# Kernel tuning notes

Hardware: AMD Instinct MI355X
Metric: run time of the kernel (lower is better)

## Reference

```python
import jax, jax.numpy as jnp
import numpy as np
import math

B, T, C, H, S = 2, 2048, 1024, 16, 16
HD = C // H
EPS = 1e-5


def setup_inputs() -> dict:
    key = jax.random.key(0)
    ks = jax.random.split(key, 20)
    sc = 1.0 / math.sqrt(C)
    inp = {
        "x": jax.random.normal(ks[0], (B, T, C), jnp.float32),
        # A_log_fwd: log(arange(1..S)) repeated over dim (as in __init__)
        "A_log": jnp.log(jnp.tile(jnp.arange(1, S + 1, dtype=jnp.float32), (C, 1))),
        # Linear weights stored (in, out); apply as x @ W + b
        "Wd": jax.random.normal(ks[1], (C, C), jnp.float32) * sc,
        "bd": jnp.full((C,), -3.0, jnp.float32),
        "WB": jax.random.normal(ks[2], (C, S), jnp.float32) * sc,
        "WC": jax.random.normal(ks[3], (C, S), jnp.float32) * sc,
        "Wq": jax.random.normal(ks[4], (C, C), jnp.float32) * sc,
        "bq": jnp.zeros((C,), jnp.float32),
        "Wk": jax.random.normal(ks[5], (C, C), jnp.float32) * sc,
        "bk": jnp.zeros((C,), jnp.float32),
        "Wv": jax.random.normal(ks[6], (C, C), jnp.float32) * sc,
        "bv": jnp.zeros((C,), jnp.float32),
        "Wx": jax.random.normal(ks[7], (C, C), jnp.float32) * sc,
        "bx": jnp.zeros((C,), jnp.float32),
        "Wo": jax.random.normal(ks[8], (C, C), jnp.float32) * sc,
        "bo": jnp.zeros((C,), jnp.float32),
        "ln_g": jnp.ones((C,), jnp.float32),
        "ln_b": jnp.zeros((C,), jnp.float32),
        "temp": jnp.full((1, H, 1, 1), 0.5, jnp.float32),
    }
    return inp


def _forward(x, A_log, Wd, bd, WB, WC, Wq, bq, Wk, bk, Wv, bv, Wx, bx, Wo, bo, ln_g, ln_b, temp):
    x_base = x @ Wx + bx                      # (B,T,C)
    delta = jax.nn.softplus(x @ Wd + bd)      # (B,T,C)
    B_mat = x @ WB                            # (B,T,S)
    C_mat = x @ WC                            # (B,T,S)
    A = -jnp.exp(A_log)                       # (C,S)

    def scan_fn(h, inp):
        xb_t, d_t, B_t, C_t = inp             # (B,C),(B,C),(B,S),(B,S)
        bar_A = jnp.exp(d_t[..., None] * A)   # (B,C,S)
        h = bar_A * h + (d_t * xb_t)[..., None] * B_t[:, None, :]
        y = jnp.einsum('bcs,bs->bc', h, C_t)
        return h, y

    h0 = jnp.zeros((B, C, S), x.dtype)
    xs = (jnp.swapaxes(x_base, 0, 1), jnp.swapaxes(delta, 0, 1),
          jnp.swapaxes(B_mat, 0, 1), jnp.swapaxes(C_mat, 0, 1))
    _, ys = jax.lax.scan(scan_fn, h0, xs)
    out_fwd = jnp.swapaxes(ys, 0, 1)          # (B,T,C)

    # LayerNorm(x_base + out_fwd)
    hyb = x_base + out_fwd
    mu = hyb.mean(-1, keepdims=True)
    var = hyb.var(-1, keepdims=True)
    hybrid = (hyb - mu) * jax.lax.rsqrt(var + EPS) * ln_g + ln_b

    def heads(W, b):
        return (hybrid @ W + b).reshape(B, T, H, HD).transpose(0, 2, 1, 3)

    Q, K, V = heads(Wq, bq), heads(Wk, bk), heads(Wv, bv)
    scores = jnp.einsum('bhqd,bhkd->bhqk', Q, K) / math.sqrt(HD)
    scores = scores * jax.nn.softplus(temp)
    mask = jnp.tril(jnp.ones((T, T), bool))
    scores = jnp.where(mask[None, None], scores, -jnp.inf)
    attn = jax.nn.softmax(scores, axis=-1)
    out = jnp.einsum('bhqk,bhkd->bhqd', attn, V).transpose(0, 2, 1, 3).reshape(B, T, C)
    return out @ Wo + bo


def reference(x, A_log, Wd, bd, WB, WC, Wq, bq, Wk, bk, Wv, bv, Wx, bx, Wo, bo, ln_g, ln_b, temp):
    return _forward(x, A_log, Wd, bd, WB, WC, Wq, bq, Wk, bk, Wv, bv, Wx, bx, Wo, bo, ln_g, ln_b, temp)
```

## Files before the change

### kernel.cpp

```cpp
#include <hip/hip_runtime.h>
#include <math.h>

#define B_  2
#define T_  2048
#define C_  1024
#define H_  16
#define S_  16
#define HD_ 64
#define NCH 32
#define CHL 64

typedef short  short8  __attribute__((ext_vector_type(8)));
typedef unsigned short ushort8 __attribute__((ext_vector_type(8)));
typedef unsigned short ushort4v __attribute__((ext_vector_type(4)));
typedef float  f32x4   __attribute__((ext_vector_type(4)));

__device__ __forceinline__ float softplus_f(float v) {
    return fmaxf(v, 0.f) + log1pf(__expf(-fabsf(v)));
}

__device__ __forceinline__ unsigned short f2bf(float x) {
    unsigned u = __float_as_uint(x);
    u += 0x7fffu + ((u >> 16) & 1u);
    return (unsigned short)(u >> 16);
}

__device__ __forceinline__ void gload16(const unsigned short* g,
                                        unsigned short* l)
{
    __builtin_amdgcn_global_load_lds(
        (const __attribute__((address_space(1))) unsigned int*)g,
        (__attribute__((address_space(3))) unsigned int*)l, 16, 0, 0);
}

__global__ __launch_bounds__(256) void cast_bf16(const float* __restrict__ in,
                                                 unsigned short* __restrict__ out,
                                                 int n4)
{
    int i = blockIdx.x * 256 + threadIdx.x;
    if (i >= n4) return;
    float4 v = ((const float4*)in)[i];
    ushort4v o = {f2bf(v.x), f2bf(v.y), f2bf(v.z), f2bf(v.w)};
    ((ushort4v*)out)[i] = o;
}

__device__ __forceinline__ void wtrans_body(const float* __restrict__ W,
                                            unsigned short* __restrict__ WT,
                                            int bx, int by, int tid)
{
    __shared__ float t[32][33];
    const int n0 = bx * 32, k0 = by * 32;
    const int tx = tid & 31, ty = tid >> 5;
#pragma unroll
    for (int p = 0; p < 4; ++p)
        t[ty + p * 8][tx] = W[(size_t)(k0 + ty + p * 8) * C_ + n0 + tx];
    __syncthreads();
#pragma unroll
    for (int p = 0; p < 4; ++p)
        WT[(size_t)(n0 + ty + p * 8) * C_ + k0 + tx] = f2bf(t[tx][ty + p * 8]);
}

__global__ __launch_bounds__(256) void wtrans(const float* __restrict__ W,
                                              unsigned short* __restrict__ WT)
{
    wtrans_body(W, WT, blockIdx.x, blockIdx.y, threadIdx.x);
}

__global__ __launch_bounds__(256) void wtrans_multi(
    const float* __restrict__ Wx, const float* __restrict__ Wd,
    const float* __restrict__ Wq, const float* __restrict__ Wk,
    const float* __restrict__ Wv,
    unsigned short* __restrict__ Astack, unsigned short* __restrict__ Wqkv)
{
    const float* src;
    unsigned short* dst;
    switch (blockIdx.z) {
        case 0: src = Wx; dst = Astack; break;
        case 1: src = Wd; dst = Astack + (size_t)1024 * 1024; break;
        case 2: src = Wq; dst = Wqkv; break;
        case 3: src = Wk; dst = Wqkv + (size_t)1024 * 1024; break;
        default: src = Wv; dst = Wqkv + (size_t)2048 * 1024; break;
    }
    wtrans_body(src, dst, blockIdx.x, blockIdx.y, threadIdx.x);
}

__global__ __launch_bounds__(256) void prep_misc(
    const float* __restrict__ WB, const float* __restrict__ WC,
    const float* __restrict__ bx, const float* __restrict__ bd,
    const float* __restrict__ bq, const float* __restrict__ bk,
    const float* __restrict__ bv,
    unsigned short* __restrict__ Astack, float* __restrict__ biasPD,
    float* __restrict__ biasQKV)
{
    int gid = blockIdx.x * 256 + threadIdx.x;
    if (gid < 32768) {
        int w = gid >> 14, rem = gid & 16383;
        int s = rem >> 10, k = rem & 1023;
        const float* src = w ? WC : WB;
        Astack[(size_t)(2048 + w * 16 + s) * 1024 + k] = f2bf(src[k * 16 + s]);
    } else {
        int id = gid - 32768;
        if (id < 2176) {
            biasPD[id] = id < 1024 ? bx[id] : (id < 2048 ? bd[id - 1024] : 0.f);
        } else {
            int id2 = id - 2176;
            if (id2 < 3072)
                biasQKV[id2] = id2 < 1024 ? bq[id2]
                             : (id2 < 2048 ? bk[id2 - 1024] : bv[id2 - 2048]);
        }
    }
}

__global__ __launch_bounds__(256) void gemm_mfma(
    const unsigned short* __restrict__ A, const unsigned short* __restrict__ Bm,
    const float* __restrict__ bias,
    void* __restrict__ outv,
    int M, int N, int K, int lda)
{
    __shared__ __align__(16) unsigned short As[4][4096];
    __shared__ __align__(16) unsigned short Bs[4][4096];

    const int tid = threadIdx.x;
    const int w = tid >> 6, lane = tid & 63;
    const int lq = lane & 15, lg = lane >> 4;
    const int wm = w >> 1, wn = w & 1;
    const int mBase = blockIdx.y * 128, nBase = blockIdx.x * 128;

    const int c0 = tid, c1 = tid + 256;
    const int rA0 = ((c0 >> 6) << 4) + (c0 & 15), kO0 = ((c0 >> 4) & 3) << 3;
    const int rA1 = ((c1 >> 6) << 4) + (c1 & 15), kO1 = ((c1 >> 4) & 3) << 3;

    const int wL0 = w * 512;
    const int wL1 = 2048 + w * 512;

    f32x4 acc[4][4];
#pragma unroll
    for (int i = 0; i < 4; ++i)
#pragma unroll
        for (int j = 0; j < 4; ++j) acc[i][j] = (f32x4){0.f, 0.f, 0.f, 0.f};

    const unsigned short* ga0 = A  + (size_t)(mBase + rA0) * lda + kO0;
    const unsigned short* ga1 = A  + (size_t)(mBase + rA1) * lda + kO1;
    const unsigned short* gb0 = Bm + (size_t)(nBase + rA0) * lda + kO0;
    const unsigned short* gb1 = Bm + (size_t)(nBase + rA1) * lda + kO1;

    #define STAGE(bufv, k0v)                               \
        do {                                               \
            gload16(ga0 + (k0v), &As[bufv][wL0]);          \
            gload16(ga1 + (k0v), &As[bufv][wL1]);          \
            gload16(gb0 + (k0v), &Bs[bufv][wL0]);          \
            gload16(gb1 + (k0v), &Bs[bufv][wL1]);          \
        } while (0)
    #define COMPUTE(bufv)                                                       \
        do {                                                                    \
            short8 a[4], b[4];                                                  \
            _Pragma("unroll")                                                   \
            for (int i = 0; i < 4; ++i)                                         \
                a[i] = *(const short8*)&As[bufv][((wm * 4 + i) * 64 + lg * 16 + lq) * 8]; \
            _Pragma("unroll")                                                   \
            for (int j = 0; j < 4; ++j)                                         \
                b[j] = *(const short8*)&Bs[bufv][((wn * 4 + j) * 64 + lg * 16 + lq) * 8]; \
            _Pragma("unroll")                                                   \
            for (int i = 0; i < 4; ++i)                                         \
                _Pragma("unroll")                                               \
                for (int j = 0; j < 4; ++j)                                     \
                    acc[i][j] = __builtin_amdgcn_mfma_f32_16x16x32_bf16(        \
                        a[i], b[j], acc[i][j], 0, 0, 0);                        \
        } while (0)
    #define WAITV4() asm volatile("s_waitcnt vmcnt(4)" ::: "memory")
    #define WAITV0() asm volatile("s_waitcnt vmcnt(0)" ::: "memory")
    #define LGKM0()  asm volatile("s_waitcnt lgkmcnt(0)" ::: "memory")
    #define STEP(cbuf, kt)                                          \
        do {                                                        \
            if ((kt) + 32 < K) WAITV4(); else WAITV0();             \
            LGKM0();                                                \
            __builtin_amdgcn_s_barrier();                           \
            if ((kt) + 64 < K) STAGE(((cbuf) + 2) & 3, (kt) + 64);  \
            COMPUTE(cbuf);                                          \
        } while (0)

    STAGE(0, 0);
    STAGE(1, 32);

    for (int k0 = 0; k0 < K; k0 += 128) {
        STEP(0, k0);
        STEP(1, k0 + 32);
        STEP(2, k0 + 64);
        STEP(3, k0 + 96);
    }
    #undef STAGE
    #undef COMPUTE
    #undef WAITV4
    #undef WAITV0
    #undef LGKM0
    #undef STEP

    float* O = (float*)outv;
#pragma unroll
    for (int j = 0; j < 4; ++j) {
        int Cg = nBase + wn * 64 + j * 16 + lq;
        float bb = bias[Cg];
#pragma unroll
        for (int i = 0; i < 4; ++i) {
            int Rb = mBase + wm * 64 + i * 16 + lg * 4;
#pragma unroll
            for (int r = 0; r < 4; ++r)
                O[(size_t)(Rb + r) * N + Cg] = acc[i][j][r] + bb;
        }
    }
}

__global__ __launch_bounds__(512, 2) void gemm_projT(
    const unsigned short* __restrict__ A, const unsigned short* __restrict__ Bm,
    const float* __restrict__ bias,
    float* __restrict__ xbaseT, float* __restrict__ deltaT,
    float* __restrict__ BmT, float* __restrict__ CmT,
    int K, int lda)
{
    __shared__ __align__(16) unsigned short AS[2][2][4096];
    __shared__ __align__(16) unsigned short BS[2][2][8192];

    const int tid = threadIdx.x;
    const int w = tid >> 6, lane = tid & 63;
    const int lq = lane & 15, lg = lane >> 4;
    const int wm = w >> 2, wn = w & 3;
    const int mBase = blockIdx.y * 128, nBase = blockIdx.x * 256;

    const int rA = ((tid >> 6) << 4) | (tid & 15);
    const int kA = ((tid >> 4) & 3) << 3;
    const unsigned short* gA = A + (size_t)(mBase + rA) * lda + kA;
    const int eA = tid * 8;
    const int c0 = tid, c1 = tid + 512;
    const int rB0 = ((c0 >> 6) << 4) | (c0 & 15), kB0 = ((c0 >> 4) & 3) << 3;
    const int rB1 = ((c1 >> 6) << 4) | (c1 & 15), kB1 = ((c1 >> 4) & 3) << 3;
    const unsigned short* gB0 = Bm + (size_t)(nBase + rB0) * lda + kB0;
    const unsigned short* gB1 = Bm + (size_t)(nBase + rB1) * lda + kB1;

    f32x4 acc[4][4];
#pragma unroll
    for (int i = 0; i < 4; ++i)
#pragma unroll
        for (int j = 0; j < 4; ++j) acc[i][j] = (f32x4){0.f, 0.f, 0.f, 0.f};

    #define STG(buf_, half_, kb_)                                             \
        do {                                                                  \
            gload16(gA  + (kb_) + (half_) * 32, &AS[buf_][half_][eA]);        \
            gload16(gB0 + (kb_) + (half_) * 32, &BS[buf_][half_][c0 * 8]);    \
            gload16(gB1 + (kb_) + (half_) * 32, &BS[buf_][half_][c1 * 8]);    \
        } while (0)
    #define WAITV6() asm volatile("s_waitcnt vmcnt(6)" ::: "memory")
    #define WAITV3() asm volatile("s_waitcnt vmcnt(3)" ::: "memory")
    #define WAITV0() asm volatile("s_waitcnt vmcnt(0)" ::: "memory")

    #define PHASE(buf_, half_, STAGE_STMT, GATE_STMT)                         \
        do {                                                                  \
            short8 a_[4], b_[4];                                              \
            _Pragma("unroll")                                                 \
            for (int i = 0; i < 4; ++i)                                       \
                a_[i] = *(const short8*)&AS[buf_][half_]                      \
                    [((wm * 4 + i) * 64 + lg * 16 + lq) * 8];                 \
            _Pragma("unroll")                                                 \
            for (int j = 0; j < 4; ++j)                                       \
                b_[j] = *(const short8*)&BS[buf_][half_]                      \
                    [((wn * 4 + j) * 64 + lg * 16 + lq) * 8];                 \
            STAGE_STMT;                                                       \
            __builtin_amdgcn_s_barrier();                                     \
            asm volatile("s_waitcnt lgkmcnt(0)" ::: "memory");                \
            __builtin_amdgcn_s_setprio(1);                                    \
            _Pragma("unroll")                                                 \
            for (int i = 0; i < 4; ++i)                                       \
                _Pragma("unroll")                                             \
                for (int j = 0; j < 4; ++j)                                   \
                    acc[i][j] = __builtin_amdgcn_mfma_f32_16x16x32_bf16(      \
                        a_[i], b_[j], acc[i][j], 0, 0, 0);                    \
            __builtin_amdgcn_s_setprio(0);                                    \
            GATE_STMT;                                                        \
            __builtin_amdgcn_s_barrier();                                     \
        } while (0)

    STG(0, 0, 0);
    STG(0, 1, 0);
    STG(1, 0, 64);
    WAITV6();
    __builtin_amdgcn_s_barrier();

    const int NT = K >> 6;
    for (int kt = 0; kt < NT; ++kt) {
        const int buf = kt & 1, nbuf = buf ^ 1;
        const int kb1 = (kt + 1) << 6, kb2 = (kt + 2) << 6;
        PHASE(buf, 0, { if (kt + 1 < NT) STG(nbuf, 1, kb1); },
              { if (kt < NT - 1) WAITV6(); else WAITV3(); });
        PHASE(buf, 1, { if (kt + 2 < NT) STG(buf, 0, kb2); },
              { if (kt < NT - 2) WAITV6();
                else if (kt == NT - 2) WAITV3(); else WAITV0(); });
    }
    #undef STG
    #undef WAITV6
    #undef WAITV3
    #undef WAITV0
    #undef PHASE

#pragma unroll
    for (int i = 0; i < 4; ++i) {
        int Rb = mBase + wm * 64 + i * 16 + lg * 4;
        if (Rb >= 2080) continue;
        float bb[4];
#pragma unroll
        for (int r = 0; r < 4; ++r) bb[r] = bias[Rb + r];
#pragma unroll
        for (int j = 0; j < 4; ++j) {
            int Cg = nBase + wn * 64 + j * 16 + lq;
            int b = Cg >> 11, t = Cg & (T_ - 1);
#pragma unroll
            for (int r = 0; r < 4; ++r) {
                int R = Rb + r;
                float v = acc[i][j][r] + bb[r];
                if (Rb < 1024) {
                    xbaseT[((size_t)b * C_ + R) * T_ + t] = v;
                } else if (Rb < 2048) {
                    deltaT[((size_t)b * C_ + (R - 1024)) * T_ + t] =
                        softplus_f(v);
                } else if (Rb < 2064) {
                    BmT[((size_t)b * S_ + (R - 2048)) * T_ + t] = v;
                } else {
                    CmT[((size_t)b * S_ + (R - 2064)) * T_ + t] = v;
                }
            }
        }
    }
}

__global__ __launch_bounds__(512, 2) void gemm_mfma256(
    const unsigned short* __restrict__ A, const unsigned short* __restrict__ Bm,
    const float* __restrict__ bias,
    void* __restrict__ outv, void* __restrict__ out2,
    void* __restrict__ out3,
    int M, int N, int K, int lda)
{
    __shared__ __align__(16) unsigned short AS[2][2][8192];
    __shared__ __align__(16) unsigned short BS[2][2][8192];

    const int tid = threadIdx.x;
    const int w = tid >> 6, lane = tid & 63;
    const int lq = lane & 15, lg = lane >> 4;
    const int wm = w >> 2, wn = w & 3;
    const int mBase = blockIdx.y * 256, nBase = blockIdx.x * 256;

    const int c0 = tid, c1 = tid + 512;
    const int r0 = ((c0 >> 6) << 4) | (c0 & 15), k0l = ((c0 >> 4) & 3) << 3;
    const int r1 = ((c1 >> 6) << 4) | (c1 & 15), k1l = ((c1 >> 4) & 3) << 3;
    const unsigned short* gA0 = A  + (size_t)(mBase + r0) * lda + k0l;
    const unsigned short* gA1 = A  + (size_t)(mBase + r1) * lda + k1l;
    const unsigned short* gB0 = Bm + (size_t)(nBase + r0) * lda + k0l;
    const unsigned short* gB1 = Bm + (size_t)(nBase + r1) * lda + k1l;

    f32x4 acc[8][4];
#pragma unroll
    for (int i = 0; i < 8; ++i)
#pragma unroll
        for (int j = 0; j < 4; ++j) acc[i][j] = (f32x4){0.f, 0.f, 0.f, 0.f};

    #define STG_A(buf_, half_, kb_)                                           \
        do {                                                                  \
            gload16(gA0 + (kb_) + (half_) * 32, &AS[buf_][half_][c0 * 8]);    \
            gload16(gA1 + (kb_) + (half_) * 32, &AS[buf_][half_][c1 * 8]);    \
        } while (0)
    #define STG_B(buf_, half_, kb_)                                           \
        do {                                                                  \
            gload16(gB0 + (kb_) + (half_) * 32, &BS[buf_][half_][c0 * 8]);    \
            gload16(gB1 + (kb_) + (half_) * 32, &BS[buf_][half_][c1 * 8]);    \
        } while (0)
    #define WAITV8() asm volatile("s_waitcnt vmcnt(8)" ::: "memory")
    #define WAITV4() asm volatile("s_waitcnt vmcnt(4)" ::: "memory")
    #define WAITV0() asm volatile("s_waitcnt vmcnt(0)" ::: "memory")

    #define PHASE(buf_, half_, qi_, STAGE_STMT, GATE_STMT)                    \
        do {                                                                  \
            short8 a_[4];                                                     \
            _Pragma("unroll")                                                 \
            for (int i = 0; i < 4; ++i)                                       \
                a_[i] = *(const short8*)&AS[buf_][half_]                      \
                    [((wm * 8 + (qi_) * 4 + i) * 64 + lg * 16 + lq) * 8];     \
            if ((qi_) == 0) {                                                 \
                _Pragma("unroll")                                             \
                for (int j = 0; j < 4; ++j)                                   \
                    bfr[j] = *(const short8*)&BS[buf_][half_]                 \
                        [((wn * 4 + j) * 64 + lg * 16 + lq) * 8];             \
            }                                                                 \
            STAGE_STMT;                                                       \
            __builtin_amdgcn_s_barrier();                                     \
            asm volatile("s_waitcnt lgkmcnt(0)" ::: "memory");                \
            __builtin_amdgcn_s_setprio(1);                                    \
            _Pragma("unroll")                                                 \
            for (int i = 0; i < 4; ++i)                                       \
                _Pragma("unroll")                                             \
                for (int j = 0; j < 4; ++j)                                   \
                    acc[(qi_) * 4 + i][j] =                                   \
                        __builtin_amdgcn_mfma_f32_16x16x32_bf16(              \
                            a_[i], bfr[j], acc[(qi_) * 4 + i][j], 0, 0, 0);   \
            __builtin_amdgcn_s_setprio(0);                                    \
            GATE_STMT;                                                        \
            __builtin_amdgcn_s_barrier();                                     \
        } while (0)

    STG_A(0, 0, 0);
    STG_B(0, 0, 0);
    STG_A(0, 1, 0);
    STG_B(0, 1, 0);
    STG_A(1, 0, 64);
    STG_B(1, 0, 64);
    WAITV8();
    __builtin_amdgcn_s_barrier();

    const int NT = K >> 6;
    for (int kt = 0; kt < NT; ++kt) {
        const int buf = kt & 1, nbuf = buf ^ 1;
        const int kb1 = (kt + 1) << 6, kb2 = (kt + 2) << 6;
        short8 bfr[4];
        PHASE(buf, 0, 0, { if (kt + 1 < NT) STG_A(nbuf, 1, kb1); }, {});
        PHASE(buf, 0, 1, { if (kt + 1 < NT) STG_B(nbuf, 1, kb1); },
              { if (kt < NT - 1) WAITV8(); else WAITV0(); });
        PHASE(buf, 1, 0, { if (kt + 2 < NT) STG_A(buf, 0, kb2); }, {});
        PHASE(buf, 1, 1, { if (kt + 2 < NT) STG_B(buf, 0, kb2); },
              { if (kt < NT - 2) WAITV8();
                else if (kt == NT - 2) WAITV4(); });
    }
    #undef STG_A
    #undef STG_B
    #undef WAITV8
    #undef WAITV4
    #undef WAITV0
    #undef PHASE

    unsigned short* Qb  = (unsigned short*)outv;
    unsigned short* Kb  = (unsigned short*)out2;
    unsigned short* VTb = (unsigned short*)out3;
#pragma unroll
    for (int j = 0; j < 4; ++j) {
        int Cg = nBase + wn * 64 + j * 16 + lq;
        int reg = Cg >> 10, c = Cg & 1023;
        int h = c >> 6, hd = c & 63;
        float bb = bias[Cg];
#pragma unroll
        for (int i = 0; i < 8; ++i) {
            int Rb = mBase + wm * 128 + i * 16 + lg * 4;
#pragma unroll
            for (int r = 0; r < 4; ++r) {
                int R = Rb + r, b = R >> 11, t = R & (T_ - 1);
                unsigned short o = f2bf(acc[i][j][r] + bb);
                if (reg == 0)
                    Qb[(((size_t)(b * H_ + h) * T_ + t) * HD_) + hd] = o;
                else if (reg == 1)
                    Kb[(((size_t)(b * H_ + h) * T_ + t) * HD_) + hd] = o;
                else
                    VTb[(((size_t)(b * H_ + h) * HD_ + hd) * T_) + t] = o;
            }
        }
    }
}

__global__ __launch_bounds__(256) void scan_partial(
    const float* __restrict__ xbaseT, const float* __restrict__ deltaT,
    const float* __restrict__ BmT, const float* __restrict__ A_log,
    float4* __restrict__ Pbuf, float4* __restrict__ Lbuf)
{
    const int tid = threadIdx.x;
    const int s4 = tid & 3;
    const int cm = tid >> 2;
    const int cg = blockIdx.x & 15;
    const int k  = (blockIdx.x >> 4) & (NCH - 1);
    const int b  = blockIdx.x >> 9;
    const int c  = cg * 64 + cm;

    float a[4];
#pragma unroll
    for (int j = 0; j < 4; ++j)
        a[j] = -__expf(A_log[c * S_ + s4 * 4 + j]);

    const int tb = k * CHL;
    const float* dp = deltaT + ((size_t)b * C_ + c) * T_ + tb;
    const float* xp = xbaseT + ((size_t)b * C_ + c) * T_ + tb;
    const float* bp = BmT + ((size_t)(b * S_ + s4 * 4)) * T_ + tb;

    float L[4] = {0.f, 0.f, 0.f, 0.f};
    float sumd = 0.f;

    float4 d4 = *(const float4*)&dp[0];
    float4 x4 = *(const float4*)&xp[0];
    float4 b4[4];
#pragma unroll
    for (int j = 0; j < 4; ++j) b4[j] = *(const float4*)&bp[(size_t)j * T_];

    for (int t0 = 0; t0 < CHL; t0 += 4) {
        const int tn = (t0 + 4 < CHL) ? t0 + 4 : t0;
        float4 d4n = *(const float4*)&dp[tn];
        float4 x4n = *(const float4*)&xp[tn];
        float4 b4n[4];
#pragma unroll
        for (int j = 0; j < 4; ++j)
            b4n[j] = *(const float4*)&bp[(size_t)j * T_ + tn];

        float dv[4] = {d4.x, d4.y, d4.z, d4.w};
        float xv[4] = {x4.x, x4.y, x4.z, x4.w};
        float bv[4][4];
#pragma unroll
        for (int j = 0; j < 4; ++j) {
            bv[j][0] = b4[j].x; bv[j][1] = b4[j].y;
            bv[j][2] = b4[j].z; bv[j][3] = b4[j].w;
        }
#pragma unroll
        for (int q = 0; q < 4; ++q) {
            float u = dv[q] * xv[q];
            sumd += dv[q];
#pragma unroll
            for (int j = 0; j < 4; ++j)
                L[j] = fmaf(__expf(dv[q] * a[j]), L[j], u * bv[j][q]);
        }
        d4 = d4n; x4 = x4n;
#pragma unroll
        for (int j = 0; j < 4; ++j) b4[j] = b4n[j];
    }
    int gid = blockIdx.x * 256 + tid;
    float4 P4 = {__expf(a[0] * sumd), __expf(a[1] * sumd),
                 __expf(a[2] * sumd), __expf(a[3] * sumd)};
    float4 L4 = {L[0], L[1], L[2], L[3]};
    Pbuf[gid] = P4;
    Lbuf[gid] = L4;
}

__global__ __launch_bounds__(256) void scan_final(
    const float* __restrict__ xbaseT, const float* __restrict__ deltaT,
    const float* __restrict__ BmT, const float* __restrict__ CmT,
    const float* __restrict__ A_log, const float4* __restrict__ Pbuf,
    const float4* __restrict__ Lbuf, float* __restrict__ hyb)
{
    const int tid = threadIdx.x;
    const int s4 = tid & 3;
    const int cm = tid >> 2;
    const int cg = blockIdx.x & 15;
    const int k  = (blockIdx.x >> 4) & (NCH - 1);
    const int b  = blockIdx.x >> 9;
    const int c  = cg * 64 + cm;

    float h[4] = {0.f, 0.f, 0.f, 0.f};
    if (k > 0) {
        const size_t g0 = (size_t)(((b * NCH) << 4) + cg) * 256 + tid;
        float4 P4 = Pbuf[g0], L4 = Lbuf[g0];
        for (int k2 = 1; k2 < k; ++k2) {
            size_t gn = g0 + (size_t)k2 * 4096;
            float4 P4n = Pbuf[gn], L4n = Lbuf[gn];
            h[0] = fmaf(P4.x, h[0], L4.x);
            h[1] = fmaf(P4.y, h[1], L4.y);
            h[2] = fmaf(P4.z, h[2], L4.z);
            h[3] = fmaf(P4.w, h[3], L4.w);
            P4 = P4n; L4 = L4n;
        }
        h[0] = fmaf(P4.x, h[0], L4.x);
        h[1] = fmaf(P4.y, h[1], L4.y);
        h[2] = fmaf(P4.z, h[2], L4.z);
        h[3] = fmaf(P4.w, h[3], L4.w);
    }

    float a[4];
#pragma unroll
    for (int j = 0; j < 4; ++j)
        a[j] = -__expf(A_log[c * S_ + s4 * 4 + j]);

    const int tb = k * CHL;
    const float* dp = deltaT + ((size_t)b * C_ + c) * T_ + tb;
    const float* xp = xbaseT + ((size_t)b * C_ + c) * T_ + tb;
    const float* bp = BmT + ((size_t)(b * S_ + s4 * 4)) * T_ + tb;
    const float* cp = CmT + ((size_t)(b * S_ + s4 * 4)) * T_ + tb;
    float* hp = hyb + ((size_t)b * T_ + tb) * C_ + c;

    float4 d4 = *(const float4*)&dp[0];
    float4 x4 = *(const float4*)&xp[0];
    float4 b4[4], c4[4];
#pragma unroll
    for (int j = 0; j < 4; ++j) {
        b4[j] = *(const float4*)&bp[(size_t)j * T_];
        c4[j] = *(const float4*)&cp[(size_t)j * T_];
    }

    for (int t0 = 0; t0 < CHL; t0 += 4) {
        const int tn = (t0 + 4 < CHL) ? t0 + 4 : t0;
        float4 d4n = *(const float4*)&dp[tn];
        float4 x4n = *(const float4*)&xp[tn];
        float4 b4n[4], c4n[4];
#pragma unroll
        for (int j = 0; j < 4; ++j) {
            b4n[j] = *(const float4*)&bp[(size_t)j * T_ + tn];
            c4n[j] = *(const float4*)&cp[(size_t)j * T_ + tn];
        }

        float dv[4] = {d4.x, d4.y, d4.z, d4.w};
        float xv[4] = {x4.x, x4.y, x4.z, x4.w};
        float bv[4][4], cv[4][4];
#pragma unroll
        for (int j = 0; j < 4; ++j) {
            bv[j][0] = b4[j].x; bv[j][1] = b4[j].y;
            bv[j][2] = b4[j].z; bv[j][3] = b4[j].w;
            cv[j][0] = c4[j].x; cv[j][1] = c4[j].y;
            cv[j][2] = c4[j].z; cv[j][3] = c4[j].w;
        }
#pragma unroll
        for (int q = 0; q < 4; ++q) {
            float u = dv[q] * xv[q];
#pragma unroll
            for (int j = 0; j < 4; ++j)
                h[j] = fmaf(__expf(dv[q] * a[j]), h[j], u * bv[j][q]);
            float y = h[0] * cv[0][q];
            y = fmaf(h[1], cv[1][q], y);
            y = fmaf(h[2], cv[2][q], y);
            y = fmaf(h[3], cv[3][q], y);
            y += __shfl_xor(y, 1, 64);
            y += __shfl_xor(y, 2, 64);
            if (s4 == 0) hp[(size_t)(t0 + q) * C_] = xv[q] + y;
        }
        d4 = d4n; x4 = x4n;
#pragma unroll
        for (int j = 0; j < 4; ++j) { b4[j] = b4n[j]; c4[j] = c4n[j]; }
    }
}

__global__ __launch_bounds__(256) void layernorm_kernel(
    const float* __restrict__ in, const float* __restrict__ g,
    const float* __restrict__ beta, unsigned short* __restrict__ out)
{
    const int row = blockIdx.x;
    const float* rp = in + (size_t)row * C_;
    const int c = threadIdx.x * 4;
    float4 v = *(const float4*)&rp[c];
    float sum = v.x + v.y + v.z + v.w;
    float sq = v.x * v.x + v.y * v.y + v.z * v.z + v.w * v.w;
#pragma unroll
    for (int off = 1; off < 64; off <<= 1) {
        sum += __shfl_xor(sum, off, 64);
        sq += __shfl_xor(sq, off, 64);
    }
    __shared__ float sS[4], sQ[4];
    int wave = threadIdx.x >> 6, lane = threadIdx.x & 63;
    if (lane == 0) { sS[wave] = sum; sQ[wave] = sq; }
    __syncthreads();
    sum = sS[0] + sS[1] + sS[2] + sS[3];
    sq = sQ[0] + sQ[1] + sQ[2] + sQ[3];
    const float mu = sum * (1.f / C_);
    const float var = sq * (1.f / C_) - mu * mu;
    const float rstd = rsqrtf(var + 1e-5f);
    float4 gg = *(const float4*)&g[c];
    float4 bb = *(const float4*)&beta[c];
    ushort4v o;
    o.x = f2bf((v.x - mu) * rstd * gg.x + bb.x);
    o.y = f2bf((v.y - mu) * rstd * gg.y + bb.y);
    o.z = f2bf((v.z - mu) * rstd * gg.z + bb.z);
    o.w = f2bf((v.w - mu) * rstd * gg.w + bb.w);
    *(ushort4v*)&out[(size_t)row * C_ + c] = o;
}

#define BKT 128
#define KP  72
#define VP  136
__global__ __launch_bounds__(256) void attn_mfma(
    const unsigned short* __restrict__ Q, const unsigned short* __restrict__ K,
    const unsigned short* __restrict__ VT, const float* __restrict__ temp,
    unsigned short* __restrict__ out)
{
    __shared__ __align__(16) unsigned short Ks[BKT * KP];
    __shared__ __align__(16) unsigned short Vs[80 * VP];
    __shared__ __align__(16) unsigned short Ps[64 * VP];

    const int tid = threadIdx.x;
    const int w = tid >> 6, lane = tid & 63;
    const int lq = lane & 15, lg = lane >> 4;
    const int p  = blockIdx.x & 15;
    const int bh = blockIdx.x >> 4;
    const int b = bh >> 4, h = bh & 15;

    const float scale = softplus_f(temp[h]) * 0.125f;
    const unsigned short* Qp = Q + (size_t)bh * T_ * HD_;
    const unsigned short* Kp = K + (size_t)bh * T_ * HD_;
    const unsigned short* Vp = VT + (size_t)bh * HD_ * T_;

    {
        int r = 64 + (tid >> 4), o = (tid & 15) * 8;
        ushort8 ones = {0x3f80, 0x3f80, 0x3f80, 0x3f80,
                        0x3f80, 0x3f80, 0x3f80, 0x3f80};
        *(ushort8*)&Vs[r * VP + o] = ones;
    }

    ushort8 kreg[4], vreg[4];
    #define LOADKV(jtv)                                                        \
        do {                                                                   \
            int kb = (jtv) * BKT;                                              \
            _Pragma("unroll")                                                  \
            for (int q2 = 0; q2 < 4; ++q2) {                                   \
                int c = tid + q2 * 256;                                        \
                kreg[q2] = *(const ushort8*)&Kp[(size_t)(kb + (c >> 3)) * HD_  \
                                                + (c & 7) * 8];                \
                vreg[q2] = *(const ushort8*)&Vp[(size_t)(c >> 4) * T_ + kb     \
                                                + (c & 15) * 8];               \
            }                                                                  \
        } while (0)

    for (int half = 0; half < 2; ++half) {
        const int qi = half ? p : (31 - p);
        const int qbase = qi * 64;
        const int nT = (qbase + 64 + BKT - 1) / BKT;

        short8 qf[2];
#pragma unroll
        for (int s = 0; s < 2; ++s)
            qf[s] = *(const short8*)&Qp[(size_t)(qbase + w * 16 + lq) * HD_
                                        + s * 32 + lg * 8];
        LOADKV(0);

        float m_i[4];
        f32x4 o[5];
#pragma unroll
        for (int r = 0; r < 4; ++r) m_i[r] = -INFINITY;
#pragma unroll
        for (int j = 0; j < 5; ++j) o[j] = (f32x4){0.f, 0.f, 0.f, 0.f};

        for (int jt = 0; jt < nT; ++jt) {
            const int kbase = jt * BKT;
            const bool last = (jt == nT - 1);
            __syncthreads();
#pragma unroll
            for (int q2 = 0; q2 < 4; ++q2) {
                int c = tid + q2 * 256;
                *(ushort8*)&Ks[(c >> 3) * KP + (c & 7) * 8] = kreg[q2];
                *(ushort8*)&Vs[(c >> 4) * VP + (c & 15) * 8] = vreg[q2];
            }
            __syncthreads();
            if (jt + 1 < nT) LOADKV(jt + 1);

            f32x4 sacc[8];
#pragma unroll
            for (int j = 0; j < 8; ++j) sacc[j] = (f32x4){0.f, 0.f, 0.f, 0.f};
#pragma unroll
            for (int s = 0; s < 2; ++s) {
#pragma unroll
                for (int j = 0; j < 8; ++j) {
                    short8 kf = *(const short8*)&Ks[(j * 16 + lq) * KP
                                                    + s * 32 + lg * 8];
                    sacc[j] = __builtin_amdgcn_mfma_f32_16x16x32_bf16(
                        qf[s], kf, sacc[j], 0, 0, 0);
                }
            }

#pragma unroll
            for (int r = 0; r < 4; ++r) {
                int qrow = qbase + w * 16 + lg * 4 + r;
                float sv[8];
#pragma unroll
                for (int j = 0; j < 8; ++j) {
                    sv[j] = sacc[j][r] * scale;
                    if (last && (kbase + j * 16 + lq > qrow)) sv[j] = -INFINITY;
                }
                float mx = sv[0];
#pragma unroll
                for (int j = 1; j < 8; ++j) mx = fmaxf(mx, sv[j]);
                mx = fmaxf(mx, __shfl_xor(mx, 1, 64));
                mx = fmaxf(mx, __shfl_xor(mx, 2, 64));
                mx = fmaxf(mx, __shfl_xor(mx, 4, 64));
                mx = fmaxf(mx, __shfl_xor(mx, 8, 64));
                float mnew = fmaxf(m_i[r], mx);
                float alpha = __expf(m_i[r] - mnew);
                m_i[r] = mnew;
#pragma unroll
                for (int j = 0; j < 5; ++j) o[j][r] *= alpha;
#pragma unroll
                for (int j = 0; j < 8; ++j)
                    Ps[(w * 16 + lg * 4 + r) * VP + j * 16 + lq] =
                        f2bf(__expf(sv[j] - mnew));
            }

#pragma unroll
            for (int s2 = 0; s2 < 4; ++s2) {
                short8 pf = *(const short8*)&Ps[(w * 16 + lq) * VP
                                                + s2 * 32 + lg * 8];
#pragma unroll
                for (int j = 0; j < 5; ++j) {
                    short8 vf = *(const short8*)&Vs[(j * 16 + lq) * VP
                                                    + s2 * 32 + lg * 8];
                    o[j] = __builtin_amdgcn_mfma_f32_16x16x32_bf16(
                        pf, vf, o[j], 0, 0, 0);
                }
            }
        }

#pragma unroll
        for (int r = 0; r < 4; ++r) {
            float inv = 1.f / o[4][r];
            int qrow = qbase + w * 16 + lg * 4 + r;
#pragma unroll
            for (int j = 0; j < 4; ++j)
                out[((size_t)(b * T_ + qrow)) * C_ + h * 64 + j * 16 + lq] =
                    f2bf(o[j][r] * inv);
        }
    }
    #undef LOADKV
}

extern "C" void kernel_launch(void* const* d_in, const int* in_sizes, int n_in,
                              void* d_out, int out_size, void* d_ws, size_t ws_size,
                              hipStream_t stream)
{
    const float* x     = (const float*)d_in[0];
    const float* A_log = (const float*)d_in[1];
    const float* Wd    = (const float*)d_in[2];
    const float* bd    = (const float*)d_in[3];
    const float* WB    = (const float*)d_in[4];
    const float* WC    = (const float*)d_in[5];
    const float* Wq    = (const float*)d_in[6];
    const float* bq    = (const float*)d_in[7];
    const float* Wk    = (const float*)d_in[8];
    const float* bk    = (const float*)d_in[9];
    const float* Wv    = (const float*)d_in[10];
    const float* bv    = (const float*)d_in[11];
    const float* Wx    = (const float*)d_in[12];
    const float* bx    = (const float*)d_in[13];
    const float* Wo    = (const float*)d_in[14];
    const float* bo    = (const float*)d_in[15];
    const float* ln_g  = (const float*)d_in[16];
    const float* ln_b  = (const float*)d_in[17];
    const float* temp  = (const float*)d_in[18];

    char* wsb = (char*)d_ws;
    const size_t MB = 1024 * 1024;
    const size_t HMB = 512 * 1024;
    unsigned short* xb      = (unsigned short*)(wsb);
    float4* Pbuf            = (float4*)(wsb);
    float4* Lbuf            = (float4*)(wsb + 4 * MB);
    unsigned short* hybrid  = (unsigned short*)(wsb);
    unsigned short* Astack  = (unsigned short*)(wsb + 8 * MB);
    float* biasPD           = (float*)(wsb + 8 * MB + (size_t)2176 * 2048);
    float* biasQKV          = biasPD + 2176;
    unsigned short* WqkvT   = (unsigned short*)(wsb + 12 * MB + HMB);
    unsigned short* WoT     = (unsigned short*)(wsb + 18 * MB + HMB);
    float* deltaT           = (float*)(wsb + 18 * MB + HMB);
    float* xbaseT           = (float*)(wsb + 34 * MB + HMB);
    float* hyb              = (float*)(wsb + 50 * MB + HMB);
    float* BmT              = (float*)(wsb + 66 * MB + HMB);
    float* CmT              = BmT + (size_t)B_ * S_ * T_;
    unsigned short* Qb      = (unsigned short*)(wsb + 20 * MB + HMB);
    unsigned short* Kb      = (unsigned short*)(wsb + 28 * MB + HMB);
    unsigned short* VTb     = (unsigned short*)(wsb + 36 * MB + HMB);
    unsigned short* attnO   = (unsigned short*)(wsb + 44 * MB + HMB);

    cast_bf16<<<4096, 256, 0, stream>>>(x, xb, (B_ * T_ * C_) / 4);
    wtrans_multi<<<dim3(32, 32, 5), 256, 0, stream>>>(Wx, Wd, Wq, Wk, Wv,
                                                      Astack, WqkvT);
    prep_misc<<<149, 256, 0, stream>>>(WB, WC, bx, bd, bq, bk, bv,
                                       Astack, biasPD, biasQKV);

    gemm_projT<<<dim3(16, 17, 1), 512, 0, stream>>>(
        Astack, xb, biasPD, xbaseT, deltaT, BmT, CmT,
        1024, 1024);

    const int scanBlocks = B_ * NCH * (C_ / 64);
    scan_partial<<<scanBlocks, 256, 0, stream>>>(xbaseT, deltaT, BmT, A_log,
                                                 Pbuf, Lbuf);
    scan_final<<<scanBlocks, 256, 0, stream>>>(xbaseT, deltaT, BmT, CmT, A_log,
                                               Pbuf, Lbuf, hyb);

    layernorm_kernel<<<B_ * T_, 256, 0, stream>>>(hyb, ln_g, ln_b, hybrid);

    gemm_mfma256<<<dim3(12, 16, 1), 512, 0, stream>>>(
        hybrid, WqkvT, biasQKV, Qb, Kb, VTb,
        4096, 3072, 1024, 1024);

    attn_mfma<<<B_ * H_ * 16, 256, 0, stream>>>(Qb, Kb, VTb, temp, attnO);

    wtrans<<<dim3(32, 32), 256, 0, stream>>>(Wo, WoT);
    gemm_mfma<<<dim3(8, 32, 1), 256, 0, stream>>>(
        attnO, WoT, bo, d_out,
        4096, 1024, 1024, 1024);
}
```

Before: 459.2 us.

## Map one channel per thread with all 16 states; stage B/C in LDS

Each scan thread now owns one channel and all 16 state dimensions, where before four threads split the states of a channel. This removes the cross-lane shuffle reduction and the redundant per-thread delta/x loads. The B and C chunk matrices are staged once per block in shared memory instead of being reloaded from global memory by every thread. The cost is a launch of only 256 blocks, which lowers parallelism, and higher register pressure from the 16-element state and coefficient arrays.

```diff
diff --git a/kernel.cpp b/kernel.cpp
--- a/kernel.cpp
+++ b/kernel.cpp
@@ -464,68 +464,76 @@
     const float* __restrict__ BmT, const float* __restrict__ A_log,
     float4* __restrict__ Pbuf, float4* __restrict__ Lbuf)
 {
+    __shared__ float bs[CHL * 16];
     const int tid = threadIdx.x;
-    const int s4 = tid & 3;
-    const int cm = tid >> 2;
-    const int cg = blockIdx.x & 15;
-    const int k  = (blockIdx.x >> 4) & (NCH - 1);
-    const int b  = blockIdx.x >> 9;
-    const int c  = cg * 64 + cm;
-
-    float a[4];
-#pragma unroll
-    for (int j = 0; j < 4; ++j)
-        a[j] = -__expf(A_log[c * S_ + s4 * 4 + j]);
-
+    const int cg = blockIdx.x & 3;
+    const int k  = (blockIdx.x >> 2) & (NCH - 1);
+    const int b  = blockIdx.x >> 7;
+    const int c  = cg * 256 + tid;
     const int tb = k * CHL;
+
+    {
+        int t0 = tid & 63, sg = (tid >> 6) << 2;
+#pragma unroll
+        for (int j = 0; j < 4; ++j)
+            bs[t0 * 16 + sg + j] =
+                BmT[((size_t)(b * S_ + sg + j)) * T_ + tb + t0];
+    }
+    float a[16];
+#pragma unroll
+    for (int sq = 0; sq < 4; ++sq) {
+        float4 a4 = *(const float4*)&A_log[(size_t)c * S_ + sq * 4];
+        a[sq * 4 + 0] = -__expf(a4.x);
+        a[sq * 4 + 1] = -__expf(a4.y);
+        a[sq * 4 + 2] = -__expf(a4.z);
+        a[sq * 4 + 3] = -__expf(a4.w);
+    }
+    __syncthreads();
+
     const float* dp = deltaT + ((size_t)b * C_ + c) * T_ + tb;
     const float* xp = xbaseT + ((size_t)b * C_ + c) * T_ + tb;
-    const float* bp = BmT + ((size_t)(b * S_ + s4 * 4)) * T_ + tb;
-
-    float L[4] = {0.f, 0.f, 0.f, 0.f};
+
+    float h[16];
+#pragma unroll
+    for (int s = 0; s < 16; ++s) h[s] = 0.f;
     float sumd = 0.f;
 
     float4 d4 = *(const float4*)&dp[0];
     float4 x4 = *(const float4*)&xp[0];
-    float4 b4[4];
-#pragma unroll
-    for (int j = 0; j < 4; ++j) b4[j] = *(const float4*)&bp[(size_t)j * T_];
-
     for (int t0 = 0; t0 < CHL; t0 += 4) {
         const int tn = (t0 + 4 < CHL) ? t0 + 4 : t0;
         float4 d4n = *(const float4*)&dp[tn];
         float4 x4n = *(const float4*)&xp[tn];
-        float4 b4n[4];
-#pragma unroll
-        for (int j = 0; j < 4; ++j)
-            b4n[j] = *(const float4*)&bp[(size_t)j * T_ + tn];
-
         float dv[4] = {d4.x, d4.y, d4.z, d4.w};
         float xv[4] = {x4.x, x4.y, x4.z, x4.w};
-        float bv[4][4];
-#pragma unroll
-        for (int j = 0; j < 4; ++j) {
-            bv[j][0] = b4[j].x; bv[j][1] = b4[j].y;
-            bv[j][2] = b4[j].z; bv[j][3] = b4[j].w;
-        }
 #pragma unroll
         for (int q = 0; q < 4; ++q) {
             float u = dv[q] * xv[q];
             sumd += dv[q];
-#pragma unroll
-            for (int j = 0; j < 4; ++j)
-                L[j] = fmaf(__expf(dv[q] * a[j]), L[j], u * bv[j][q]);
+            float bv[16];
+#pragma unroll
+            for (int sq = 0; sq < 4; ++sq) {
+                float4 b4 = *(const float4*)&bs[(t0 + q) * 16 + sq * 4];
+                bv[sq * 4 + 0] = b4.x; bv[sq * 4 + 1] = b4.y;
+                bv[sq * 4 + 2] = b4.z; bv[sq * 4 + 3] = b4.w;
+            }
+#pragma unroll
+            for (int s = 0; s < 16; ++s)
+                h[s] = fmaf(__expf(dv[q] * a[s]), h[s], u * bv[s]);
         }
         d4 = d4n; x4 = x4n;
-#pragma unroll
-        for (int j = 0; j < 4; ++j) b4[j] = b4n[j];
-    }
-    int gid = blockIdx.x * 256 + tid;
-    float4 P4 = {__expf(a[0] * sumd), __expf(a[1] * sumd),
-                 __expf(a[2] * sumd), __expf(a[3] * sumd)};
-    float4 L4 = {L[0], L[1], L[2], L[3]};
-    Pbuf[gid] = P4;
-    Lbuf[gid] = L4;
+    }
+
+    const size_t base = ((size_t)((b * NCH + k) << 10) + c) * 4;
+#pragma unroll
+    for (int sq = 0; sq < 4; ++sq) {
+        float4 P4 = {__expf(a[sq * 4 + 0] * sumd), __expf(a[sq * 4 + 1] * sumd),
+                     __expf(a[sq * 4 + 2] * sumd), __expf(a[sq * 4 + 3] * sumd)};
+        float4 L4 = {h[sq * 4 + 0], h[sq * 4 + 1],
+                     h[sq * 4 + 2], h[sq * 4 + 3]};
+        Pbuf[base + sq] = P4;
+        Lbuf[base + sq] = L4;
+    }
 }
 
 __global__ __launch_bounds__(256) void scan_final(
@@ -534,92 +542,91 @@
     const float* __restrict__ A_log, const float4* __restrict__ Pbuf,
     const float4* __restrict__ Lbuf, float* __restrict__ hyb)
 {
+    __shared__ float bs[CHL * 16];
+    __shared__ float cs[CHL * 16];
     const int tid = threadIdx.x;
-    const int s4 = tid & 3;
-    const int cm = tid >> 2;
-    const int cg = blockIdx.x & 15;
-    const int k  = (blockIdx.x >> 4) & (NCH - 1);
-    const int b  = blockIdx.x >> 9;
-    const int c  = cg * 64 + cm;
-
-    float h[4] = {0.f, 0.f, 0.f, 0.f};
-    if (k > 0) {
-        const size_t g0 = (size_t)(((b * NCH) << 4) + cg) * 256 + tid;
-        float4 P4 = Pbuf[g0], L4 = Lbuf[g0];
-        for (int k2 = 1; k2 < k; ++k2) {
-            size_t gn = g0 + (size_t)k2 * 4096;
-            float4 P4n = Pbuf[gn], L4n = Lbuf[gn];
-            h[0] = fmaf(P4.x, h[0], L4.x);
-            h[1] = fmaf(P4.y, h[1], L4.y);
-            h[2] = fmaf(P4.z, h[2], L4.z);
-            h[3] = fmaf(P4.w, h[3], L4.w);
-            P4 = P4n; L4 = L4n;
-        }
-        h[0] = fmaf(P4.x, h[0], L4.x);
-        h[1] = fmaf(P4.y, h[1], L4.y);
-        h[2] = fmaf(P4.z, h[2], L4.z);
-        h[3] = fmaf(P4.w, h[3], L4.w);
-    }
-
-    float a[4];
-#pragma unroll
-    for (int j = 0; j < 4; ++j)
-        a[j] = -__expf(A_log[c * S_ + s4 * 4 + j]);
-
+    const int cg = blockIdx.x & 3;
+    const int k  = (blockIdx.x >> 2) & (NCH - 1);
+    const int b  = blockIdx.x >> 7;
+    const int c  = cg * 256 + tid;
     const int tb = k * CHL;
+
+    {
+        int t0 = tid & 63, sg = (tid >> 6) << 2;
+#pragma unroll
+        for (int j = 0; j < 4; ++j) {
+            bs[t0 * 16 + sg + j] =
+                BmT[((size_t)(b * S_ + sg + j)) * T_ + tb + t0];
+            cs[t0 * 16 + sg + j] =
+                CmT[((size_t)(b * S_ + sg + j)) * T_ + tb + t0];
+        }
+    }
+    float a[16];
+#pragma unroll
+    for (int sq = 0; sq < 4; ++sq) {
+        float4 a4 = *(const float4*)&A_log[(size_t)c * S_ + sq * 4];
+        a[sq * 4 + 0] = -__expf(a4.x);
+        a[sq * 4 + 1] = -__expf(a4.y);
+        a[sq * 4 + 2] = -__expf(a4.z);
+        a[sq * 4 + 3] = -__expf(a4.w);
+    }
+
+    float h[16];
+#pragma unroll
+    for (int s = 0; s < 16; ++s) h[s] = 0.f;
+    for (int k2 = 0; k2 < k; ++k2) {
+        const size_t b2 = ((size_t)((b * NCH + k2) << 10) + c) * 4;
+#pragma unroll
+        for (int sq = 0; sq < 4; ++sq) {
+            float4 P4 = Pbuf[b2 + sq];
+            float4 L4 = Lbuf[b2 + sq];
+            h[sq * 4 + 0] = fmaf(P4.x, h[sq * 4 + 0], L4.x);
+            h[sq * 4 + 1] = fmaf(P4.y, h[sq * 4 + 1], L4.y);
+            h[sq * 4 + 2] = fmaf(P4.z, h[sq * 4 + 2], L4.z);
+            h[sq * 4 + 3] = fmaf(P4.w, h[sq * 4 + 3], L4.w);
+        }
+    }
+    __syncthreads();
+
     const float* dp = deltaT + ((size_t)b * C_ + c) * T_ + tb;
     const float* xp = xbaseT + ((size_t)b * C_ + c) * T_ + tb;
-    const float* bp = BmT + ((size_t)(b * S_ + s4 * 4)) * T_ + tb;
-    const float* cp = CmT + ((size_t)(b * S_ + s4 * 4)) * T_ + tb;
     float* hp = hyb + ((size_t)b * T_ + tb) * C_ + c;
 
     float4 d4 = *(const float4*)&dp[0];
     float4 x4 = *(const float4*)&xp[0];
-    float4 b4[4], c4[4];
-#pragma unroll
-    for (int j = 0; j < 4; ++j) {
-        b4[j] = *(const float4*)&bp[(size_t)j * T_];
-        c4[j] = *(const float4*)&cp[(size_t)j * T_];
-    }
-
     for (int t0 = 0; t0 < CHL; t0 += 4) {
         const int tn = (t0 + 4 < CHL) ? t0 + 4 : t0;
         float4 d4n = *(const float4*)&dp[tn];
         float4 x4n = *(const float4*)&xp[tn];
-        float4 b4n[4], c4n[4];
-#pragma unroll
-        for (int j = 0; j < 4; ++j) {
-            b4n[j] = *(const float4*)&bp[(size_t)j * T_ + tn];
-            c4n[j] = *(const float4*)&cp[(size_t)j * T_ + tn];
-        }
-
         float dv[4] = {d4.x, d4.y, d4.z, d4.w};
         float xv[4] = {x4.x, x4.y, x4.z, x4.w};
-        float bv[4][4], cv[4][4];
-#pragma unroll
-        for (int j = 0; j < 4; ++j) {
-            bv[j][0] = b4[j].x; bv[j][1] = b4[j].y;
-            bv[j][2] = b4[j].z; bv[j][3] = b4[j].w;
-            cv[j][0] = c4[j].x; cv[j][1] = c4[j].y;
-            cv[j][2] = c4[j].z; cv[j][3] = c4[j].w;
-        }
 #pragma unroll
         for (int q = 0; q < 4; ++q) {
             float u = dv[q] * xv[q];
-#pragma unroll
-            for (int j = 0; j < 4; ++j)
-                h[j] = fmaf(__expf(dv[q] * a[j]), h[j], u * bv[j][q]);
-            float y = h[0] * cv[0][q];
-            y = fmaf(h[1], cv[1][q], y);
-            y = fmaf(h[2], cv[2][q], y);
-            y = fmaf(h[3], cv[3][q], y);
-            y += __shfl_xor(y, 1, 64);
-            y += __shfl_xor(y, 2, 64);
-            if (s4 == 0) hp[(size_t)(t0 + q) * C_] = xv[q] + y;
+            float bv[16], cv[16];
+#pragma unroll
+            for (int sq = 0; sq < 4; ++sq) {
+                float4 b4 = *(const float4*)&bs[(t0 + q) * 16 + sq * 4];
+                float4 c4 = *(const float4*)&cs[(t0 + q) * 16 + sq * 4];
+                bv[sq * 4 + 0] = b4.x; bv[sq * 4 + 1] = b4.y;
+                bv[sq * 4 + 2] = b4.z; bv[sq * 4 + 3] = b4.w;
+                cv[sq * 4 + 0] = c4.x; cv[sq * 4 + 1] = c4.y;
+                cv[sq * 4 + 2] = c4.z; cv[sq * 4 + 3] = c4.w;
+            }
+#pragma unroll
+            for (int s = 0; s < 16; ++s)
+                h[s] = fmaf(__expf(dv[q] * a[s]), h[s], u * bv[s]);
+            float y0 = 0.f, y1 = 0.f, y2 = 0.f, y3 = 0.f;
+#pragma unroll
+            for (int sq = 0; sq < 4; ++sq) {
+                y0 = fmaf(h[sq * 4 + 0], cv[sq * 4 + 0], y0);
+                y1 = fmaf(h[sq * 4 + 1], cv[sq * 4 + 1], y1);
+                y2 = fmaf(h[sq * 4 + 2], cv[sq * 4 + 2], y2);
+                y3 = fmaf(h[sq * 4 + 3], cv[sq * 4 + 3], y3);
+            }
+            hp[(size_t)(t0 + q) * C_] = xv[q] + ((y0 + y1) + (y2 + y3));
         }
         d4 = d4n; x4 = x4n;
-#pragma unroll
-        for (int j = 0; j < 4; ++j) { b4[j] = b4n[j]; c4[j] = c4n[j]; }
     }
 }
 
@@ -858,7 +865,7 @@
         Astack, xb, biasPD, xbaseT, deltaT, BmT, CmT,
         1024, 1024);
 
-    const int scanBlocks = B_ * NCH * (C_ / 64);
+    const int scanBlocks = B_ * NCH * 4;
     scan_partial<<<scanBlocks, 256, 0, stream>>>(xbaseT, deltaT, BmT, A_log,
                                                  Pbuf, Lbuf);
     scan_final<<<scanBlocks, 256, 0, stream>>>(xbaseT, deltaT, BmT, CmT, A_log,
```

New measurement: 408.2 us. 1.12x faster.
